# Performance work log

Hardware: AMD Instinct MI355X
Metric: run time of the kernel (lower is better)

The kernel has to match this reference:

```python
import jax, jax.numpy as jnp
import numpy as np
import math

D_MODEL = 512
H = 8
DK = D_MODEL // H  # 64
B, S = 2, 4096


def setup_inputs() -> dict:
    key = jax.random.key(0)
    ks = jax.random.split(key, 11)
    sc = 1.0 / math.sqrt(D_MODEL)
    return {
        "query": jax.random.normal(ks[0], (B, S, D_MODEL), jnp.float32),
        "key": jax.random.normal(ks[1], (B, S, D_MODEL), jnp.float32),
        "value": jax.random.normal(ks[2], (B, S, D_MODEL), jnp.float32),
        "Wq": jax.random.normal(ks[3], (D_MODEL, D_MODEL), jnp.float32) * sc,
        "bq": jnp.zeros((D_MODEL,), jnp.float32),
        "Wk": jax.random.normal(ks[4], (D_MODEL, D_MODEL), jnp.float32) * sc,
        "bk": jnp.zeros((D_MODEL,), jnp.float32),
        "Wv": jax.random.normal(ks[5], (D_MODEL, D_MODEL), jnp.float32) * sc,
        "bv": jnp.zeros((D_MODEL,), jnp.float32),
        "Wo": jax.random.normal(ks[6], (D_MODEL, D_MODEL), jnp.float32) * sc,
        "bo": jnp.zeros((D_MODEL,), jnp.float32),
    }


def reference(query, key, value, Wq, bq, Wk, bk, Wv, bv, Wo, bo):
    b = query.shape[0]
    # projections; W stored [in, out]
    def proj(x, W, bias):
        y = x @ W + bias                      # [B,S,h*dk]
        return y.reshape(b, -1, H, DK).transpose(0, 2, 1, 3)  # [B,h,S,dk]

    q = proj(query, Wq, bq)
    k = proj(key, Wk, bk)
    v = proj(value, Wv, bv)
    scores = jnp.einsum("bhqd,bhkd->bhqk", q, k) / math.sqrt(DK)
    attn = jax.nn.softmax(scores, axis=-1)    # [B,h,Sq,Sk]
    ctx = jnp.einsum("bhqk,bhkd->bhqd", attn, v)
    ctx = ctx.transpose(0, 2, 1, 3).reshape(b, -1, H * DK)  # [B,S,d_model]
    return ctx @ Wo + bo
```

## Files before the change

### kernel.cpp

```cpp
#include <hip/hip_runtime.h>
#include <hip/hip_bf16.h>

#define DM   512
#define HEADS 8
#define DKH  64
#define BATCH 2
#define SEQ  4096

typedef float  f32x4  __attribute__((ext_vector_type(4)));
typedef float  f32x16 __attribute__((ext_vector_type(16)));
typedef __bf16 bf16x8 __attribute__((ext_vector_type(8)));
typedef __bf16 bf16x4 __attribute__((ext_vector_type(4)));
typedef __bf16 bf16x2 __attribute__((ext_vector_type(2)));

static __device__ __forceinline__ f32x4 mfma16(bf16x8 a, bf16x8 b, f32x4 c) {
    return __builtin_amdgcn_mfma_f32_16x16x32_bf16(a, b, c, 0, 0, 0);
}
static __device__ __forceinline__ f32x16 mfma32(bf16x8 a, bf16x8 b, f32x16 c) {
    return __builtin_amdgcn_mfma_f32_32x32x16_bf16(a, b, c, 0, 0, 0);
}

#define GLD16(gp, lp) __builtin_amdgcn_global_load_lds( \
    (const __attribute__((address_space(1))) void*)(gp), \
    (__attribute__((address_space(3))) void*)(lp), 16, 0, 0)

#define WAITVM(n) asm volatile("s_waitcnt vmcnt(" #n ")" ::: "memory")

static __device__ __forceinline__ void barrier_sync() {
    __builtin_amdgcn_sched_barrier(0);
    asm volatile("" ::: "memory");
    __builtin_amdgcn_s_barrier();
    asm volatile("" ::: "memory");
    __builtin_amdgcn_sched_barrier(0);
}

struct Cvt3 { const float* s[3]; __bf16* d[3]; };

__global__ __launch_bounds__(256) void convert_x3(Cvt3 a) {
    const float* s = a.s[blockIdx.y];
    __bf16* d = a.d[blockIdx.y];
    const size_t i = ((size_t)blockIdx.x * 256 + threadIdx.x) * 8;
    f32x4 f0 = *(const f32x4*)&s[i];
    f32x4 f1 = *(const f32x4*)&s[i + 4];
    bf16x8 v;
    v[0] = (__bf16)f0[0]; v[1] = (__bf16)f0[1]; v[2] = (__bf16)f0[2]; v[3] = (__bf16)f0[3];
    v[4] = (__bf16)f1[0]; v[5] = (__bf16)f1[1]; v[6] = (__bf16)f1[2]; v[7] = (__bf16)f1[3];
    *(bf16x8*)&d[i] = v;
}

struct WtAll { const float* W[4]; __bf16* Wt[4]; };

__global__ __launch_bounds__(256) void wt_convert_all(WtAll a) {
    const float* W = a.W[blockIdx.z];
    __bf16* Wt = a.Wt[blockIdx.z];
    __shared__ float tile[32][33];
    const int tx = threadIdx.x & 31, ty = threadIdx.x >> 5;
    const int nb = blockIdx.x * 32, kb = blockIdx.y * 32;
#pragma unroll
    for (int i = 0; i < 4; ++i)
        tile[ty + 8 * i][tx] = W[(size_t)(kb + ty + 8 * i) * DM + nb + tx];
    __syncthreads();
#pragma unroll
    for (int i = 0; i < 4; ++i)
        Wt[(size_t)(nb + ty + 8 * i) * DM + kb + tx] = (__bf16)tile[tx][ty + 8 * i];
}

struct Ptr3 { const __bf16* A; const __bf16* Bt; const float* bias; void* Out; float ascale; int vt; };
struct GemmArgs { Ptr3 p[3]; };

template <bool OUT_BF16, int BN>
__global__ __launch_bounds__(256) void gemm_tile(GemmArgs args) {
    constexpr int BGLD = BN / 32;
    constexpr int NJ   = BN / 32;
    constexpr int NT   = DM / 64;
    __shared__ __bf16 Al[2][128][64];
    __shared__ __bf16 Bl[2][BN][64];
    const Ptr3 P = args.p[blockIdx.z];
    const int tid = threadIdx.x;
    const int lane = tid & 63, wid = tid >> 6;
    const int lq = lane & 15, hi = lane >> 4;
    const int m0 = blockIdx.x * 128, n0 = blockIdx.y * BN;
    const int wm = (wid >> 1) * 64, wn = (wid & 1) * (BN / 2);

    const int lrow = lane >> 3, lslot = lane & 7;
    const __bf16* gaP[4];
#pragma unroll
    for (int i = 0; i < 4; ++i) {
        const int r = wid * 32 + i * 8 + lrow;
        const int s = lslot ^ ((r ^ (r >> 3)) & 7);
        gaP[i] = P.A + (size_t)(m0 + r) * DM + s * 8;
    }
    const __bf16* gbP[BGLD];
#pragma unroll
    for (int i = 0; i < BGLD; ++i) {
        const int r = wid * (BN / 4) + i * 8 + lrow;
        const int s = lslot ^ ((r ^ (r >> 3)) & 7);
        gbP[i] = P.Bt + (size_t)(n0 + r) * DM + s * 8;
    }
    auto stage = [&](int kt, int buf) {
        const int k0 = kt * 64;
#pragma unroll
        for (int i = 0; i < 4; ++i)
            GLD16(gaP[i] + k0, &Al[buf][wid * 32 + i * 8][0]);
#pragma unroll
        for (int i = 0; i < BGLD; ++i)
            GLD16(gbP[i] + k0, &Bl[buf][wid * (BN / 4) + i * 8][0]);
    };

    int baseA[4], swA[4];
#pragma unroll
    for (int i = 0; i < 4; ++i) {
        const int r = wm + i * 16 + lq;
        baseA[i] = r * 128;
        swA[i] = (((r ^ (r >> 3)) & 7) << 4);
    }
    int baseB[NJ], swB[NJ];
#pragma unroll
    for (int j = 0; j < NJ; ++j) {
        const int r = wn + j * 16 + lq;
        baseB[j] = r * 128;
        swB[j] = (((r ^ (r >> 3)) & 7) << 4);
    }

    f32x4 acc[4][NJ] = {};

    stage(0, 0);
    stage(1, 1);
    for (int kt = 0; kt < NT; ++kt) {
        const int cur = kt & 1;
        if (kt + 1 < NT) {
            if (BN == 128) { WAITVM(8); } else { WAITVM(6); }
        } else { WAITVM(0); }
        barrier_sync();
        const char* Ab = (const char*)&Al[cur][0][0];
        const char* Bb = (const char*)&Bl[cur][0][0];
        __builtin_amdgcn_s_setprio(1);
#pragma unroll
        for (int ks = 0; ks < 2; ++ks) {
            const int off = ks * 64 + hi * 16;
            bf16x8 af[4], bfv[NJ];
#pragma unroll
            for (int i = 0; i < 4; ++i)
                af[i] = *(const bf16x8*)(Ab + baseA[i] + (off ^ swA[i]));
#pragma unroll
            for (int j = 0; j < NJ; ++j)
                bfv[j] = *(const bf16x8*)(Bb + baseB[j] + (off ^ swB[j]));
#pragma unroll
            for (int i = 0; i < 4; ++i)
#pragma unroll
                for (int j = 0; j < NJ; ++j)
                    acc[i][j] = mfma16(af[i], bfv[j], acc[i][j]);
        }
        __builtin_amdgcn_s_setprio(0);
        if (kt + 2 < NT) {
            barrier_sync();
            stage(kt + 2, cur);
        }
    }

    const float* bias = P.bias;
    const float asc = P.ascale;
    if (OUT_BF16 && P.vt) {
#pragma unroll
        for (int j = 0; j < NJ; ++j) {
            const int n = n0 + wn + j * 16 + lq;
            const int head = n >> 6, dk = n & 63;
            const float bv = bias[n];
#pragma unroll
            for (int i = 0; i < 4; ++i) {
                const int m = m0 + wm + i * 16 + hi * 4;
                const int b = m >> 12, q = m & (SEQ - 1);
                bf16x4 vv;
#pragma unroll
                for (int r = 0; r < 4; ++r) vv[r] = (__bf16)((acc[i][j][r] + bv) * asc);
                *(bf16x4*)&((__bf16*)P.Out)[((size_t)((b * HEADS + head) * DKH + dk)) * SEQ + q] = vv;
            }
        }
    } else {
#pragma unroll
        for (int j = 0; j < NJ; ++j) {
            const int n = n0 + wn + j * 16 + lq;
            const float bv = bias[n];
#pragma unroll
            for (int i = 0; i < 4; ++i) {
#pragma unroll
                for (int r = 0; r < 4; ++r) {
                    const int m = m0 + wm + i * 16 + hi * 4 + r;
                    const float v = (acc[i][j][r] + bv) * asc;
                    if (OUT_BF16) ((__bf16*)P.Out)[(size_t)m * DM + n] = (__bf16)v;
                    else          ((float*)P.Out)[(size_t)m * DM + n] = v;
                }
            }
        }
    }
}

template <bool SPLIT>
__global__ __launch_bounds__(256, 4) void flash_attn5(const __bf16* __restrict__ Qp,
                                                      const __bf16* __restrict__ Kp,
                                                      const __bf16* __restrict__ Vt,
                                                      __bf16* __restrict__ O0,
                                                      __bf16* __restrict__ O1,
                                                      float* __restrict__ MLM,
                                                      float* __restrict__ MLL) {
    __shared__ __bf16 Kl[2][64][64];
    __shared__ __bf16 Vl[2][64][64];
    __shared__ float  Lbuf[4][32];

    const int tid = threadIdx.x, lane = tid & 63, w = tid >> 6;
    const int c = lane & 31, h = lane >> 5;

    constexpr int NBLK = 32 * 16 * (SPLIT ? 2 : 1);
    constexpr int CPX = NBLK / 8;
    int fid = blockIdx.x + 32 * (blockIdx.y + 16 * blockIdx.z);
    fid = (fid & 7) * CPX + (fid >> 3);
    const int qt = fid & 31;
    const int bh = (fid >> 5) & 15;
    const int zz = SPLIT ? (fid >> 9) : 0;

    const int b = bh >> 3, hd = bh & 7;
    const int qbase = qt * 128 + w * 32;
    const int kvoff = SPLIT ? zz * (SEQ / 2) : 0;
    const int NT = SPLIT ? (SEQ / 2) / 64 : SEQ / 64;

    bf16x8 qf[4];
#pragma unroll
    for (int t = 0; t < 4; ++t)
        qf[t] = *(const bf16x8*)&Qp[(size_t)(b * SEQ + qbase + c) * DM + hd * DKH + 16 * t + 8 * h];

    const int r0 = w * 16 + (lane >> 3);
    const int r1 = r0 + 8;
    const int s0 = (lane & 7) ^ ((r0 ^ (r0 >> 3)) & 7);
    const int s1 = (lane & 7) ^ ((r1 ^ (r1 >> 3)) & 7);
    const __bf16* kg0 = Kp + (size_t)(b * SEQ + kvoff + r0) * DM + hd * DKH + s0 * 8;
    const __bf16* kg1 = Kp + (size_t)(b * SEQ + kvoff + r1) * DM + hd * DKH + s1 * 8;
    const __bf16* vg0 = Vt + (size_t)(bh * DKH + r0) * SEQ + kvoff + s0 * 8;
    const __bf16* vg1 = Vt + (size_t)(bh * DKH + r1) * SEQ + kvoff + s1 * 8;

    const int swz0 = (c ^ (c >> 3)) & 7;
    const int swz1 = ((32 + c) ^ ((32 + c) >> 3)) & 7;
    const int rowb0 = c * 128, rowb1 = (32 + c) * 128;
    const char* kb = (const char*)&Kl[0][0][0];
    const char* vb = (const char*)&Vl[0][0][0];

    auto stage = [&](int t, int buf) {
        const size_t ko = (size_t)t * 64 * DM, vo = (size_t)t * 64;
        GLD16(kg0 + ko, &Kl[buf][w * 16][0]);
        GLD16(kg1 + ko, &Kl[buf][w * 16 + 8][0]);
        GLD16(vg0 + vo, &Vl[buf][w * 16][0]);
        GLD16(vg1 + vo, &Vl[buf][w * 16 + 8][0]);
    };

    bf16x8 vone;
#pragma unroll
    for (int j = 0; j < 8; ++j) vone[j] = (__bf16)1.0f;

    f32x16 acc0 = {}, acc1 = {}, lacc = {};
    float m_run = -__builtin_inff();

    stage(0, 0);
    __syncthreads();

    for (int t = 0; t < NT; ++t) {
        const int cur = t & 1;
        if (t + 1 < NT) stage(t + 1, cur ^ 1);
        const char* kc = kb + cur * 8192;
        const char* vc = vb + cur * 8192;

        f32x16 sa = {}, sb = {};
        __builtin_amdgcn_s_setprio(1);
#pragma unroll
        for (int tt = 0; tt < 4; ++tt) {
            bf16x8 kf0 = *(const bf16x8*)(kc + rowb0 + (((2 * tt + h) ^ swz0) << 4));
            sa = mfma32(kf0, qf[tt], sa);
            bf16x8 kf1 = *(const bf16x8*)(kc + rowb1 + (((2 * tt + h) ^ swz1) << 4));
            sb = mfma32(kf1, qf[tt], sb);
        }
        __builtin_amdgcn_s_setprio(0);

        float mx = fmaxf(sa[0], sa[1]);
#pragma unroll
        for (int r = 2; r < 16; r += 2) mx = fmaxf(mx, fmaxf(sa[r], sa[r + 1]));
#pragma unroll
        for (int r = 0; r < 16; r += 2) mx = fmaxf(mx, fmaxf(sb[r], sb[r + 1]));
        mx = fmaxf(mx, __shfl_xor(mx, 32));
        if (!__all(mx <= m_run + 8.f)) {
            const float mnew = fmaxf(m_run, mx);
            const float al = __builtin_amdgcn_exp2f(m_run - mnew);
            m_run = mnew;
            if (lane < 32) Lbuf[w][lane] = al;
#pragma unroll
            for (int r = 0; r < 16; ++r) {
                const float a2 = Lbuf[w][(r & 3) + 8 * (r >> 2) + 4 * h];
                acc0[r] *= a2; acc1[r] *= a2; lacc[r] *= a2;
            }
        }

        int ua[4][2], ub[4][2];
#pragma unroll
        for (int q4 = 0; q4 < 4; ++q4) {
            float p0 = __builtin_amdgcn_exp2f(sa[4 * q4 + 0] - m_run);
            float p1 = __builtin_amdgcn_exp2f(sa[4 * q4 + 1] - m_run);
            float p2 = __builtin_amdgcn_exp2f(sa[4 * q4 + 2] - m_run);
            float p3 = __builtin_amdgcn_exp2f(sa[4 * q4 + 3] - m_run);
            bf16x2 t0; t0[0] = (__bf16)p0; t0[1] = (__bf16)p1;
            bf16x2 t1; t1[0] = (__bf16)p2; t1[1] = (__bf16)p3;
            ua[q4][0] = __builtin_bit_cast(int, t0);
            ua[q4][1] = __builtin_bit_cast(int, t1);
        }
#pragma unroll
        for (int q4 = 0; q4 < 4; ++q4) {
            float p0 = __builtin_amdgcn_exp2f(sb[4 * q4 + 0] - m_run);
            float p1 = __builtin_amdgcn_exp2f(sb[4 * q4 + 1] - m_run);
            float p2 = __builtin_amdgcn_exp2f(sb[4 * q4 + 2] - m_run);
            float p3 = __builtin_amdgcn_exp2f(sb[4 * q4 + 3] - m_run);
            bf16x2 t0; t0[0] = (__bf16)p0; t0[1] = (__bf16)p1;
            bf16x2 t1; t1[0] = (__bf16)p2; t1[1] = (__bf16)p3;
            ub[q4][0] = __builtin_bit_cast(int, t0);
            ub[q4][1] = __builtin_bit_cast(int, t1);
        }

#pragma unroll
        for (int tg = 0; tg < 4; ++tg) {
            int x0, y0, x1, y1;
            if (tg < 2) {
                x0 = ua[2 * tg][0]; y0 = ua[2 * tg + 1][0];
                x1 = ua[2 * tg][1]; y1 = ua[2 * tg + 1][1];
            } else {
                x0 = ub[2 * (tg - 2)][0]; y0 = ub[2 * (tg - 2) + 1][0];
                x1 = ub[2 * (tg - 2)][1]; y1 = ub[2 * (tg - 2) + 1][1];
            }
            asm("v_permlane32_swap_b32 %0, %1" : "+v"(x0), "+v"(y0));
            asm("v_permlane32_swap_b32 %0, %1" : "+v"(x1), "+v"(y1));
            union { int i4[4]; bf16x8 v; } pf;
            pf.i4[0] = x0; pf.i4[1] = x1; pf.i4[2] = y0; pf.i4[3] = y1;
            bf16x8 vf0 = *(const bf16x8*)(vc + rowb0 + (((2 * tg + h) ^ swz0) << 4));
            bf16x8 vf1 = *(const bf16x8*)(vc + rowb1 + (((2 * tg + h) ^ swz1) << 4));
            __builtin_amdgcn_s_setprio(1);
            acc0 = mfma32(pf.v, vf0, acc0);
            acc1 = mfma32(pf.v, vf1, acc1);
            lacc = mfma32(pf.v, vone, lacc);
            __builtin_amdgcn_s_setprio(0);
        }
        __syncthreads();
    }

    if (SPLIT) {
        __bf16* pp = zz ? O1 : O0;
#pragma unroll
        for (int r = 0; r < 16; ++r) {
            const int qr = (r & 3) + 8 * (r >> 2) + 4 * h;
            const size_t off = (size_t)(b * SEQ + qbase + qr) * DM + hd * DKH;
            pp[off + c]      = (__bf16)acc0[r];
            pp[off + 32 + c] = (__bf16)acc1[r];
        }
        const int zo = zz * 16 + bh;
        if (h == 0) MLM[(size_t)zo * SEQ + qbase + c] = m_run;
        if (c == 0) {
#pragma unroll
            for (int r = 0; r < 16; ++r) {
                const int qr = (r & 3) + 8 * (r >> 2) + 4 * h;
                MLL[(size_t)zo * SEQ + qbase + qr] = lacc[r];
            }
        }
    } else {
        __bf16* outp = O0 + (size_t)(b * SEQ + qbase) * DM + hd * DKH;
#pragma unroll
        for (int r = 0; r < 16; ++r) {
            const int qr = (r & 3) + 8 * (r >> 2) + 4 * h;
            const float li = 1.f / lacc[r];
            outp[(size_t)qr * DM + c]      = (__bf16)(acc0[r] * li);
            outp[(size_t)qr * DM + 32 + c] = (__bf16)(acc1[r] * li);
        }
    }
}

__global__ __launch_bounds__(256) void combine(const __bf16* __restrict__ P0,
                                               const __bf16* __restrict__ P1,
                                               const float* __restrict__ MLM,
                                               const float* __restrict__ MLL,
                                               __bf16* __restrict__ Ctx) {
    const int row = blockIdx.x;
    const int b = row >> 12, q = row & (SEQ - 1);
    const int col = threadIdx.x * 2;
    const int head = col >> 6;
    const int bh = b * HEADS + head;
    const float m0 = MLM[(size_t)bh * SEQ + q];
    const float m1 = MLM[(size_t)(16 + bh) * SEQ + q];
    const float l0 = MLL[(size_t)bh * SEQ + q];
    const float l1 = MLL[(size_t)(16 + bh) * SEQ + q];
    const float m = fmaxf(m0, m1);
    const float e0 = __builtin_amdgcn_exp2f(m0 - m);
    const float e1 = __builtin_amdgcn_exp2f(m1 - m);
    const float inv = 1.f / (l0 * e0 + l1 * e1);
    const float f0 = e0 * inv, f1 = e1 * inv;
    const size_t idx = (size_t)row * DM + col;
    bf16x2 a = *(const bf16x2*)&P0[idx];
    bf16x2 bb = *(const bf16x2*)&P1[idx];
    bf16x2 o;
    o[0] = (__bf16)((float)a[0] * f0 + (float)bb[0] * f1);
    o[1] = (__bf16)((float)a[1] * f0 + (float)bb[1] * f1);
    *(bf16x2*)&Ctx[idx] = o;
}

extern "C" void kernel_launch(void* const* d_in, const int* in_sizes, int n_in,
                              void* d_out, int out_size, void* d_ws, size_t ws_size,
                              hipStream_t stream) {
    (void)in_sizes; (void)n_in; (void)out_size;
    const float* query = (const float*)d_in[0];
    const float* key_  = (const float*)d_in[1];
    const float* value = (const float*)d_in[2];
    const float* Wq = (const float*)d_in[3];
    const float* bq = (const float*)d_in[4];
    const float* Wk = (const float*)d_in[5];
    const float* bk = (const float*)d_in[6];
    const float* Wv = (const float*)d_in[7];
    const float* bv = (const float*)d_in[8];
    const float* Wo = (const float*)d_in[9];
    const float* bo = (const float*)d_in[10];

    char* ws = (char*)d_ws;
    const size_t WSZ = (size_t)512 * 1024;
    const size_t XSZ = (size_t)8 * 1024 * 1024;
    const float QSC = 0.125f * 1.4426950408889634f;
    if (ws_size < 4 * WSZ + 7 * XSZ) return;

    __bf16* Wtq = (__bf16*)(ws);
    __bf16* Wtk = (__bf16*)(ws + WSZ);
    __bf16* Wtv = (__bf16*)(ws + 2 * WSZ);
    __bf16* Wto = (__bf16*)(ws + 3 * WSZ);
    char* xb = ws + 4 * WSZ;
    __bf16* Qb = (__bf16*)(xb);
    __bf16* Kb = (__bf16*)(xb + XSZ);
    __bf16* Vb = (__bf16*)(xb + 2 * XSZ);
    __bf16* Qp = (__bf16*)(xb + 3 * XSZ);
    __bf16* Kp = (__bf16*)(xb + 4 * XSZ);
    __bf16* Vt = (__bf16*)(xb + 5 * XSZ);
    __bf16* Ctx = (__bf16*)(xb + 6 * XSZ);
    __bf16* P0 = Qb;
    __bf16* P1 = Kb;
    float* MLM = (float*)Vb;
    float* MLL = MLM + 2 * 16 * SEQ;

    Cvt3 cv;
    cv.s[0] = query; cv.s[1] = key_; cv.s[2] = value;
    cv.d[0] = Qb; cv.d[1] = Kb; cv.d[2] = Vb;
    convert_x3<<<dim3(2048, 3), 256, 0, stream>>>(cv);

    WtAll wa;
    wa.W[0] = Wq; wa.W[1] = Wk; wa.W[2] = Wv; wa.W[3] = Wo;
    wa.Wt[0] = Wtq; wa.Wt[1] = Wtk; wa.Wt[2] = Wtv; wa.Wt[3] = Wto;
    wt_convert_all<<<dim3(16, 16, 4), 256, 0, stream>>>(wa);

    GemmArgs qa;
    qa.p[0] = {Qb, Wtq, bq, Qp, QSC, 0};
    qa.p[1] = {Kb, Wtk, bk, Kp, 1.0f, 0};
    qa.p[2] = {Vb, Wtv, bv, Vt, 1.0f, 1};
    gemm_tile<true, 128><<<dim3(64, 4, 3), 256, 0, stream>>>(qa);

    flash_attn5<true><<<dim3(SEQ / 128, BATCH * HEADS, 2), 256, 0, stream>>>(
        Qp, Kp, Vt, P0, P1, MLM, MLL);

    combine<<<dim3(BATCH * SEQ), 256, 0, stream>>>(P0, P1, MLM, MLL, Ctx);

    GemmArgs oa;
    oa.p[0] = {Ctx, Wto, bo, d_out, 1.0f, 0};
    oa.p[1] = oa.p[0]; oa.p[2] = oa.p[0];
    gemm_tile<false, 64><<<dim3(64, 8, 1), 256, 0, stream>>>(oa);
}
```

Measured before the change: 256.0 us.

## Fuse split-KV combine into output GEMM, merge prep kernels, compute row sums on VALU

Merges the input conversion and weight transpose kernels into one launch. The split-KV combine step now happens inside the output projection GEMM, which rescales and merges the two partial contexts while loading its A tile, so the Ctx buffer and the separate combine kernel go away. In flash attention the softmax row sum is now accumulated with scalar adds and a shuffle instead of an extra MFMA against a vector of ones. The new output GEMM loses double buffering and recomputes the combine factors once per N-tile (8 times), which may stall its loads.

Measured after the change: 243.8 us. 4.7% less time.

```diff
diff --git a/kernel.cpp b/kernel.cpp
--- a/kernel.cpp
+++ b/kernel.cpp
@@ -34,45 +34,44 @@
     __builtin_amdgcn_sched_barrier(0);
 }
 
-struct Cvt3 { const float* s[3]; __bf16* d[3]; };
-
-__global__ __launch_bounds__(256) void convert_x3(Cvt3 a) {
-    const float* s = a.s[blockIdx.y];
-    __bf16* d = a.d[blockIdx.y];
-    const size_t i = ((size_t)blockIdx.x * 256 + threadIdx.x) * 8;
-    f32x4 f0 = *(const f32x4*)&s[i];
-    f32x4 f1 = *(const f32x4*)&s[i + 4];
-    bf16x8 v;
-    v[0] = (__bf16)f0[0]; v[1] = (__bf16)f0[1]; v[2] = (__bf16)f0[2]; v[3] = (__bf16)f0[3];
-    v[4] = (__bf16)f1[0]; v[5] = (__bf16)f1[1]; v[6] = (__bf16)f1[2]; v[7] = (__bf16)f1[3];
-    *(bf16x8*)&d[i] = v;
-}
-
-struct WtAll { const float* W[4]; __bf16* Wt[4]; };
-
-__global__ __launch_bounds__(256) void wt_convert_all(WtAll a) {
-    const float* W = a.W[blockIdx.z];
-    __bf16* Wt = a.Wt[blockIdx.z];
+struct PrepArgs { const float* s[3]; __bf16* d[3]; const float* W[4]; __bf16* Wt[4]; };
+
+__global__ __launch_bounds__(256) void prep_all(PrepArgs a) {
     __shared__ float tile[32][33];
-    const int tx = threadIdx.x & 31, ty = threadIdx.x >> 5;
-    const int nb = blockIdx.x * 32, kb = blockIdx.y * 32;
-#pragma unroll
-    for (int i = 0; i < 4; ++i)
-        tile[ty + 8 * i][tx] = W[(size_t)(kb + ty + 8 * i) * DM + nb + tx];
-    __syncthreads();
-#pragma unroll
-    for (int i = 0; i < 4; ++i)
-        Wt[(size_t)(nb + ty + 8 * i) * DM + kb + tx] = (__bf16)tile[tx][ty + 8 * i];
+    const int bid = blockIdx.x;
+    if (bid < 6144) {
+        const int t = bid >> 11, cb = bid & 2047;
+        const float* s = a.s[t];
+        __bf16* d = a.d[t];
+        const size_t i = ((size_t)cb * 256 + threadIdx.x) * 8;
+        f32x4 f0 = *(const f32x4*)&s[i];
+        f32x4 f1 = *(const f32x4*)&s[i + 4];
+        bf16x8 v;
+        v[0] = (__bf16)f0[0]; v[1] = (__bf16)f0[1]; v[2] = (__bf16)f0[2]; v[3] = (__bf16)f0[3];
+        v[4] = (__bf16)f1[0]; v[5] = (__bf16)f1[1]; v[6] = (__bf16)f1[2]; v[7] = (__bf16)f1[3];
+        *(bf16x8*)&d[i] = v;
+    } else {
+        const int r = bid - 6144;
+        const int wsel = r >> 8, tl = r & 255;
+        const float* W = a.W[wsel];
+        __bf16* Wt = a.Wt[wsel];
+        const int nb = (tl & 15) * 32, kb = (tl >> 4) * 32;
+        const int tx = threadIdx.x & 31, ty = threadIdx.x >> 5;
+#pragma unroll
+        for (int i = 0; i < 4; ++i)
+            tile[ty + 8 * i][tx] = W[(size_t)(kb + ty + 8 * i) * DM + nb + tx];
+        __syncthreads();
+#pragma unroll
+        for (int i = 0; i < 4; ++i)
+            Wt[(size_t)(nb + ty + 8 * i) * DM + kb + tx] = (__bf16)tile[tx][ty + 8 * i];
+    }
 }
 
 struct Ptr3 { const __bf16* A; const __bf16* Bt; const float* bias; void* Out; float ascale; int vt; };
 struct GemmArgs { Ptr3 p[3]; };
 
-template <bool OUT_BF16, int BN>
-__global__ __launch_bounds__(256) void gemm_tile(GemmArgs args) {
-    constexpr int BGLD = BN / 32;
-    constexpr int NJ   = BN / 32;
-    constexpr int NT   = DM / 64;
+__global__ __launch_bounds__(256) void gemm_qkv(GemmArgs args) {
+    constexpr int BN = 128, BGLD = 4, NJ = 4, NT = DM / 64;
     __shared__ __bf16 Al[2][128][64];
     __shared__ __bf16 Bl[2][BN][64];
     const Ptr3 P = args.p[blockIdx.z];
@@ -128,9 +127,7 @@
     stage(1, 1);
     for (int kt = 0; kt < NT; ++kt) {
         const int cur = kt & 1;
-        if (kt + 1 < NT) {
-            if (BN == 128) { WAITVM(8); } else { WAITVM(6); }
-        } else { WAITVM(0); }
+        if (kt + 1 < NT) { WAITVM(8); } else { WAITVM(0); }
         barrier_sync();
         const char* Ab = (const char*)&Al[cur][0][0];
         const char* Bb = (const char*)&Bl[cur][0][0];
@@ -160,7 +157,7 @@
 
     const float* bias = P.bias;
     const float asc = P.ascale;
-    if (OUT_BF16 && P.vt) {
+    if (P.vt) {
 #pragma unroll
         for (int j = 0; j < NJ; ++j) {
             const int n = n0 + wn + j * 16 + lq;
@@ -186,17 +183,14 @@
 #pragma unroll
                 for (int r = 0; r < 4; ++r) {
                     const int m = m0 + wm + i * 16 + hi * 4 + r;
-                    const float v = (acc[i][j][r] + bv) * asc;
-                    if (OUT_BF16) ((__bf16*)P.Out)[(size_t)m * DM + n] = (__bf16)v;
-                    else          ((float*)P.Out)[(size_t)m * DM + n] = v;
+                    ((__bf16*)P.Out)[(size_t)m * DM + n] = (__bf16)((acc[i][j][r] + bv) * asc);
                 }
             }
         }
     }
 }
 
-template <bool SPLIT>
-__global__ __launch_bounds__(256, 4) void flash_attn5(const __bf16* __restrict__ Qp,
+__global__ __launch_bounds__(256, 4) void flash_attn6(const __bf16* __restrict__ Qp,
                                                       const __bf16* __restrict__ Kp,
                                                       const __bf16* __restrict__ Vt,
                                                       __bf16* __restrict__ O0,
@@ -210,18 +204,18 @@
     const int tid = threadIdx.x, lane = tid & 63, w = tid >> 6;
     const int c = lane & 31, h = lane >> 5;
 
-    constexpr int NBLK = 32 * 16 * (SPLIT ? 2 : 1);
+    constexpr int NBLK = 32 * 16 * 2;
     constexpr int CPX = NBLK / 8;
     int fid = blockIdx.x + 32 * (blockIdx.y + 16 * blockIdx.z);
     fid = (fid & 7) * CPX + (fid >> 3);
     const int qt = fid & 31;
     const int bh = (fid >> 5) & 15;
-    const int zz = SPLIT ? (fid >> 9) : 0;
+    const int zz = fid >> 9;
 
     const int b = bh >> 3, hd = bh & 7;
     const int qbase = qt * 128 + w * 32;
-    const int kvoff = SPLIT ? zz * (SEQ / 2) : 0;
-    const int NT = SPLIT ? (SEQ / 2) / 64 : SEQ / 64;
+    const int kvoff = zz * (SEQ / 2);
+    const int NT = (SEQ / 2) / 64;
 
     bf16x8 qf[4];
 #pragma unroll
@@ -251,12 +245,8 @@
         GLD16(vg1 + vo, &Vl[buf][w * 16 + 8][0]);
     };
 
-    bf16x8 vone;
-#pragma unroll
-    for (int j = 0; j < 8; ++j) vone[j] = (__bf16)1.0f;
-
-    f32x16 acc0 = {}, acc1 = {}, lacc = {};
-    float m_run = -__builtin_inff();
+    f32x16 acc0 = {}, acc1 = {};
+    float m_run = -__builtin_inff(), l_run = 0.f;
 
     stage(0, 0);
     __syncthreads();
@@ -288,14 +278,16 @@
             const float mnew = fmaxf(m_run, mx);
             const float al = __builtin_amdgcn_exp2f(m_run - mnew);
             m_run = mnew;
+            l_run *= al;
             if (lane < 32) Lbuf[w][lane] = al;
 #pragma unroll
             for (int r = 0; r < 16; ++r) {
                 const float a2 = Lbuf[w][(r & 3) + 8 * (r >> 2) + 4 * h];
-                acc0[r] *= a2; acc1[r] *= a2; lacc[r] *= a2;
+                acc0[r] *= a2; acc1[r] *= a2;
             }
         }
 
+        float ls = 0.f;
         int ua[4][2], ub[4][2];
 #pragma unroll
         for (int q4 = 0; q4 < 4; ++q4) {
@@ -303,6 +295,7 @@
             float p1 = __builtin_amdgcn_exp2f(sa[4 * q4 + 1] - m_run);
             float p2 = __builtin_amdgcn_exp2f(sa[4 * q4 + 2] - m_run);
             float p3 = __builtin_amdgcn_exp2f(sa[4 * q4 + 3] - m_run);
+            ls += p0 + p1 + p2 + p3;
             bf16x2 t0; t0[0] = (__bf16)p0; t0[1] = (__bf16)p1;
             bf16x2 t1; t1[0] = (__bf16)p2; t1[1] = (__bf16)p3;
             ua[q4][0] = __builtin_bit_cast(int, t0);
@@ -314,11 +307,14 @@
             float p1 = __builtin_amdgcn_exp2f(sb[4 * q4 + 1] - m_run);
             float p2 = __builtin_amdgcn_exp2f(sb[4 * q4 + 2] - m_run);
             float p3 = __builtin_amdgcn_exp2f(sb[4 * q4 + 3] - m_run);
+            ls += p0 + p1 + p2 + p3;
             bf16x2 t0; t0[0] = (__bf16)p0; t0[1] = (__bf16)p1;
             bf16x2 t1; t1[0] = (__bf16)p2; t1[1] = (__bf16)p3;
             ub[q4][0] = __builtin_bit_cast(int, t0);
             ub[q4][1] = __builtin_bit_cast(int, t1);
         }
+        ls += __shfl_xor(ls, 32);
+        l_run += ls;
 
 #pragma unroll
         for (int tg = 0; tg < 4; ++tg) {
@@ -339,68 +335,146 @@
             __builtin_amdgcn_s_setprio(1);
             acc0 = mfma32(pf.v, vf0, acc0);
             acc1 = mfma32(pf.v, vf1, acc1);
-            lacc = mfma32(pf.v, vone, lacc);
             __builtin_amdgcn_s_setprio(0);
         }
         __syncthreads();
     }
 
-    if (SPLIT) {
-        __bf16* pp = zz ? O1 : O0;
-#pragma unroll
-        for (int r = 0; r < 16; ++r) {
-            const int qr = (r & 3) + 8 * (r >> 2) + 4 * h;
-            const size_t off = (size_t)(b * SEQ + qbase + qr) * DM + hd * DKH;
-            pp[off + c]      = (__bf16)acc0[r];
-            pp[off + 32 + c] = (__bf16)acc1[r];
-        }
-        const int zo = zz * 16 + bh;
-        if (h == 0) MLM[(size_t)zo * SEQ + qbase + c] = m_run;
-        if (c == 0) {
-#pragma unroll
-            for (int r = 0; r < 16; ++r) {
-                const int qr = (r & 3) + 8 * (r >> 2) + 4 * h;
-                MLL[(size_t)zo * SEQ + qbase + qr] = lacc[r];
+    __bf16* pp = zz ? O1 : O0;
+#pragma unroll
+    for (int r = 0; r < 16; ++r) {
+        const int qr = (r & 3) + 8 * (r >> 2) + 4 * h;
+        const size_t off = (size_t)(b * SEQ + qbase + qr) * DM + hd * DKH;
+        pp[off + c]      = (__bf16)acc0[r];
+        pp[off + 32 + c] = (__bf16)acc1[r];
+    }
+    const int zo = zz * 16 + bh;
+    if (h == 0) {
+        MLM[(size_t)zo * SEQ + qbase + c] = m_run;
+        MLL[(size_t)zo * SEQ + qbase + c] = l_run;
+    }
+}
+
+__global__ __launch_bounds__(256) void gemm_out(const __bf16* __restrict__ P0,
+                                                const __bf16* __restrict__ P1,
+                                                const float* __restrict__ MLM,
+                                                const float* __restrict__ MLL,
+                                                const __bf16* __restrict__ Bt,
+                                                const float* __restrict__ bias,
+                                                float* __restrict__ Out) {
+    constexpr int BN = 64, NJ = 2, NT = DM / 64;
+    __shared__ __bf16 Al[128][64];
+    __shared__ __bf16 Bl[BN][64];
+    const int tid = threadIdx.x;
+    const int lane = tid & 63, wid = tid >> 6;
+    const int lq = lane & 15, hi = lane >> 4;
+    const int m0 = blockIdx.x * 128, n0 = blockIdx.y * BN;
+    const int wm = (wid >> 1) * 64, wn = (wid & 1) * (BN / 2);
+
+    const int lrow = lane >> 3, lslot = lane & 7;
+    int arow[4]; size_t abase[4];
+#pragma unroll
+    for (int i = 0; i < 4; ++i) {
+        arow[i] = wid * 32 + i * 8 + lrow;
+        abase[i] = (size_t)(m0 + arow[i]) * DM + lslot * 8;
+    }
+    const __bf16* gbP[2];
+#pragma unroll
+    for (int i = 0; i < 2; ++i) {
+        const int r = wid * 16 + i * 8 + lrow;
+        const int s = lslot ^ ((r ^ (r >> 3)) & 7);
+        gbP[i] = Bt + (size_t)(n0 + r) * DM + s * 8;
+    }
+
+    int baseA[4], swA[4];
+#pragma unroll
+    for (int i = 0; i < 4; ++i) {
+        const int r = wm + i * 16 + lq;
+        baseA[i] = r * 128;
+        swA[i] = (((r ^ (r >> 3)) & 7) << 4);
+    }
+    int baseB[NJ], swB[NJ];
+#pragma unroll
+    for (int j = 0; j < NJ; ++j) {
+        const int r = wn + j * 16 + lq;
+        baseB[j] = r * 128;
+        swB[j] = (((r ^ (r >> 3)) & 7) << 4);
+    }
+
+    f32x4 acc[4][NJ] = {};
+
+    for (int kt = 0; kt < NT; ++kt) {
+        const int k0 = kt * 64;
+        bf16x8 aw[4];
+#pragma unroll
+        for (int i = 0; i < 4; ++i) {
+            const int m = m0 + arow[i];
+            const int b = m >> 12, q = m & (SEQ - 1);
+            const int bh = b * HEADS + kt;
+            bf16x8 a0 = *(const bf16x8*)&P0[abase[i] + k0];
+            bf16x8 a1 = *(const bf16x8*)&P1[abase[i] + k0];
+            const float mv0 = MLM[(size_t)bh * SEQ + q];
+            const float mv1 = MLM[(size_t)(16 + bh) * SEQ + q];
+            const float lv0 = MLL[(size_t)bh * SEQ + q];
+            const float lv1 = MLL[(size_t)(16 + bh) * SEQ + q];
+            const float mm = fmaxf(mv0, mv1);
+            const float e0 = __builtin_amdgcn_exp2f(mv0 - mm);
+            const float e1 = __builtin_amdgcn_exp2f(mv1 - mm);
+            const float inv = 1.f / (lv0 * e0 + lv1 * e1);
+            const float f0 = e0 * inv, f1 = e1 * inv;
+            bf16x8 o;
+#pragma unroll
+            for (int j = 0; j < 8; ++j)
+                o[j] = (__bf16)((float)a0[j] * f0 + (float)a1[j] * f1);
+            aw[i] = o;
+        }
+        if (kt) __syncthreads();
+#pragma unroll
+        for (int i = 0; i < 2; ++i)
+            GLD16(gbP[i] + k0, &Bl[wid * 16 + i * 8][0]);
+#pragma unroll
+        for (int i = 0; i < 4; ++i) {
+            const int r = arow[i];
+            char* dst = (char*)&Al[0][0] + r * 128 + ((lslot ^ ((r ^ (r >> 3)) & 7)) << 4);
+            *(bf16x8*)dst = aw[i];
+        }
+        __syncthreads();
+
+        const char* Ab = (const char*)&Al[0][0];
+        const char* Bb = (const char*)&Bl[0][0];
+        __builtin_amdgcn_s_setprio(1);
+#pragma unroll
+        for (int ks = 0; ks < 2; ++ks) {
+            const int off = ks * 64 + hi * 16;
+            bf16x8 af[4], bfv[NJ];
+#pragma unroll
+            for (int i = 0; i < 4; ++i)
+                af[i] = *(const bf16x8*)(Ab + baseA[i] + (off ^ swA[i]));
+#pragma unroll
+            for (int j = 0; j < NJ; ++j)
+                bfv[j] = *(const bf16x8*)(Bb + baseB[j] + (off ^ swB[j]));
+#pragma unroll
+            for (int i = 0; i < 4; ++i)
+#pragma unroll
+                for (int j = 0; j < NJ; ++j)
+                    acc[i][j] = mfma16(af[i], bfv[j], acc[i][j]);
+        }
+        __builtin_amdgcn_s_setprio(0);
+    }
+
+#pragma unroll
+    for (int j = 0; j < NJ; ++j) {
+        const int n = n0 + wn + j * 16 + lq;
+        const float bv = bias[n];
+#pragma unroll
+        for (int i = 0; i < 4; ++i) {
+#pragma unroll
+            for (int r = 0; r < 4; ++r) {
+                const int m = m0 + wm + i * 16 + hi * 4 + r;
+                Out[(size_t)m * DM + n] = acc[i][j][r] + bv;
             }
         }
-    } else {
-        __bf16* outp = O0 + (size_t)(b * SEQ + qbase) * DM + hd * DKH;
-#pragma unroll
-        for (int r = 0; r < 16; ++r) {
-            const int qr = (r & 3) + 8 * (r >> 2) + 4 * h;
-            const float li = 1.f / lacc[r];
-            outp[(size_t)qr * DM + c]      = (__bf16)(acc0[r] * li);
-            outp[(size_t)qr * DM + 32 + c] = (__bf16)(acc1[r] * li);
-        }
-    }
-}
-
-__global__ __launch_bounds__(256) void combine(const __bf16* __restrict__ P0,
-                                               const __bf16* __restrict__ P1,
-                                               const float* __restrict__ MLM,
-                                               const float* __restrict__ MLL,
-                                               __bf16* __restrict__ Ctx) {
-    const int row = blockIdx.x;
-    const int b = row >> 12, q = row & (SEQ - 1);
-    const int col = threadIdx.x * 2;
-    const int head = col >> 6;
-    const int bh = b * HEADS + head;
-    const float m0 = MLM[(size_t)bh * SEQ + q];
-    const float m1 = MLM[(size_t)(16 + bh) * SEQ + q];
-    const float l0 = MLL[(size_t)bh * SEQ + q];
-    const float l1 = MLL[(size_t)(16 + bh) * SEQ + q];
-    const float m = fmaxf(m0, m1);
-    const float e0 = __builtin_amdgcn_exp2f(m0 - m);
-    const float e1 = __builtin_amdgcn_exp2f(m1 - m);
-    const float inv = 1.f / (l0 * e0 + l1 * e1);
-    const float f0 = e0 * inv, f1 = e1 * inv;
-    const size_t idx = (size_t)row * DM + col;
-    bf16x2 a = *(const bf16x2*)&P0[idx];
-    bf16x2 bb = *(const bf16x2*)&P1[idx];
-    bf16x2 o;
-    o[0] = (__bf16)((float)a[0] * f0 + (float)bb[0] * f1);
-    o[1] = (__bf16)((float)a[1] * f0 + (float)bb[1] * f1);
-    *(bf16x2*)&Ctx[idx] = o;
+    }
 }
 
 extern "C" void kernel_launch(void* const* d_in, const int* in_sizes, int n_in,
@@ -436,35 +510,26 @@
     __bf16* Qp = (__bf16*)(xb + 3 * XSZ);
     __bf16* Kp = (__bf16*)(xb + 4 * XSZ);
     __bf16* Vt = (__bf16*)(xb + 5 * XSZ);
-    __bf16* Ctx = (__bf16*)(xb + 6 * XSZ);
     __bf16* P0 = Qb;
     __bf16* P1 = Kb;
     float* MLM = (float*)Vb;
     float* MLL = MLM + 2 * 16 * SEQ;
 
-    Cvt3 cv;
-    cv.s[0] = query; cv.s[1] = key_; cv.s[2] = value;
-    cv.d[0] = Qb; cv.d[1] = Kb; cv.d[2] = Vb;
-    convert_x3<<<dim3(2048, 3), 256, 0, stream>>>(cv);
-
-    WtAll wa;
-    wa.W[0] = Wq; wa.W[1] = Wk; wa.W[2] = Wv; wa.W[3] = Wo;
-    wa.Wt[0] = Wtq; wa.Wt[1] = Wtk; wa.Wt[2] = Wtv; wa.Wt[3] = Wto;
-    wt_convert_all<<<dim3(16, 16, 4), 256, 0, stream>>>(wa);
+    PrepArgs pa;
+    pa.s[0] = query; pa.s[1] = key_; pa.s[2] = value;
+    pa.d[0] = Qb; pa.d[1] = Kb; pa.d[2] = Vb;
+    pa.W[0] = Wq; pa.W[1] = Wk; pa.W[2] = Wv; pa.W[3] = Wo;
+    pa.Wt[0] = Wtq; pa.Wt[1] = Wtk; pa.Wt[2] = Wtv; pa.Wt[3] = Wto;
+    prep_all<<<dim3(7168), 256, 0, stream>>>(pa);
 
     GemmArgs qa;
     qa.p[0] = {Qb, Wtq, bq, Qp, QSC, 0};
     qa.p[1] = {Kb, Wtk, bk, Kp, 1.0f, 0};
     qa.p[2] = {Vb, Wtv, bv, Vt, 1.0f, 1};
-    gemm_tile<true, 128><<<dim3(64, 4, 3), 256, 0, stream>>>(qa);
-
-    flash_attn5<true><<<dim3(SEQ / 128, BATCH * HEADS, 2), 256, 0, stream>>>(
+    gemm_qkv<<<dim3(64, 4, 3), 256, 0, stream>>>(qa);
+
+    flash_attn6<<<dim3(SEQ / 128, BATCH * HEADS, 2), 256, 0, stream>>>(
         Qp, Kp, Vt, P0, P1, MLM, MLL);
 
-    combine<<<dim3(BATCH * SEQ), 256, 0, stream>>>(P0, P1, MLM, MLL, Ctx);
-
-    GemmArgs oa;
-    oa.p[0] = {Ctx, Wto, bo, d_out, 1.0f, 0};
-    oa.p[1] = oa.p[0]; oa.p[2] = oa.p[0];
-    gemm_tile<false, 64><<<dim3(64, 8, 1), 256, 0, stream>>>(oa);
-}
+    gemm_out<<<dim3(64, 8), 256, 0, stream>>>(P0, P1, MLM, MLL, Wto, bo, (float*)d_out);
+}
```
